# Kernel tuning notes

Hardware: AMD Instinct MI355X
Metric: run time of the kernel (lower is better)

## Reference

```python
import jax, jax.numpy as jnp
import numpy as np

KERNEL = 3
STRIDE = 1
PAD = 1


def setup_inputs() -> dict:
    key = jax.random.key(0)
    k1, k2 = jax.random.split(key)
    x = jax.random.normal(k1, (16, 32, 512, 512), dtype=jnp.float32)
    # original init: torch.rand(O, I, k, k) / (k*k)
    kernels = jax.random.uniform(k2, (32, 32, KERNEL, KERNEL), dtype=jnp.float32) / (KERNEL * KERNEL)
    return {"x": x, "kernels": kernels}


def reference(x, kernels):
    # Equivalent math to the unfold+einsum im2col conv2d: pad, extract kxk
    # windows with stride, contract over (in_channels, kh, kw).
    # Expressed as a direct convolution (cross-correlation), which is the
    # same computation without materializing the 6D window tensor.
    out = jax.lax.conv_general_dilated(
        x, kernels,
        window_strides=(STRIDE, STRIDE),
        padding=((PAD, PAD), (PAD, PAD)),
        dimension_numbers=("NCHW", "OIHW", "NCHW"),
    )
    return out  # [B, out_channels, H_out, W_out]
```

## Files before the change

kernel.cpp:

```cpp
#include <hip/hip_runtime.h>
#include <hip/hip_bf16.h>

typedef __attribute__((ext_vector_type(8))) short bf16x8;
typedef __attribute__((ext_vector_type(4))) float f32x4;
typedef __attribute__((ext_vector_type(4))) unsigned int u32x4;

#define HH 512
#define WWD 512
#define HW (HH * WWD)
#define TW 64
#define HALO_W 66
#define ROWS 10
#define NPIX (ROWS * HALO_W)
#define XBYTES (NPIX * 64)
#define WOFF XBYTES
#define WBYTES (9 * 4 * 32 * 16)
#define DUMMY (WOFF + WBYTES)
#define NITER 32

__device__ __forceinline__ unsigned short f2bf(float f) {
    unsigned u = __builtin_bit_cast(unsigned, f);
    u += 0x7FFFu + ((u >> 16) & 1u);
    return (unsigned short)(u >> 16);
}

__device__ __forceinline__ void issue4(const float* __restrict__ xb, int row0, int w0,
                                       float (&sv)[3][8]) {
    #pragma unroll
    for (int k = 0; k < 3; ++k) {
        int u = threadIdx.x + k * 512;
        int g = u / 384, r = u - g * 384, hh = r / 96, ww = r - hh * 96;
        int wwc = ww < 66 ? ww : 65;
        int row = row0 + hh, cl = w0 + wwc - 1;
        bool ok = (ww < 66) & ((unsigned)row < 512u) & ((unsigned)cl < 512u);
        int rowc = row < 0 ? 0 : (row > 511 ? 511 : row);
        int clc  = cl  < 0 ? 0 : (cl  > 511 ? 511 : cl);
        const float* src = xb + (size_t)(g * 8) * HW + rowc * WWD + clc;
        #pragma unroll
        for (int j = 0; j < 8; ++j) { float v = src[(size_t)j * HW]; sv[k][j] = ok ? v : 0.f; }
    }
}

__device__ __forceinline__ void write4(char* smem, int wsb, float (&sv)[3][8]) {
    #pragma unroll
    for (int k = 0; k < 3; ++k) {
        int u = threadIdx.x + k * 512;
        int g = u / 384, r = u - g * 384, hh = r / 96, ww = r - hh * 96;
        int slot = wsb + hh; if (slot >= ROWS) slot -= ROWS;
        int byte = (ww < 66) ? (g * NPIX + slot * HALO_W + ww) * 16
                             : (DUMMY + (threadIdx.x & 63) * 16);
        unsigned q0 = (unsigned)f2bf(sv[k][0]) | ((unsigned)f2bf(sv[k][1]) << 16);
        unsigned q1 = (unsigned)f2bf(sv[k][2]) | ((unsigned)f2bf(sv[k][3]) << 16);
        unsigned q2 = (unsigned)f2bf(sv[k][4]) | ((unsigned)f2bf(sv[k][5]) << 16);
        unsigned q3 = (unsigned)f2bf(sv[k][6]) | ((unsigned)f2bf(sv[k][7]) << 16);
        u32x4 q = { q0, q1, q2, q3 };
        *(u32x4*)(smem + byte) = q;
    }
}

template<int WAITN, bool ISS, bool WR, bool BAR>
__device__ __forceinline__ void conv_body(char* smem, const float* __restrict__ xb,
                                          float* __restrict__ ob,
                                          float (&cur)[3][8], float (&nxt)[3][8],
                                          int srb, int rowbase, int issrow, int w0,
                                          int wv, int col16, int g4) {
    if (ISS) {
        issue4(xb, issrow, w0, nxt);
        __builtin_amdgcn_sched_barrier(0);
    }
    if constexpr (WAITN == 28) asm volatile("s_waitcnt vmcnt(28)" ::: "memory");
    else if constexpr (WAITN == 4) asm volatile("s_waitcnt vmcnt(4)" ::: "memory");
    if constexpr (WAITN != 63) __builtin_amdgcn_sched_barrier(0);

    if (WR) {
        int wsb = srb + 6; if (wsb >= ROWS) wsb -= ROWS;
        write4(smem, wsb, cur);
    }

    f32x4 acc[2][2];
    {
        f32x4 z = {0.f, 0.f, 0.f, 0.f};
        acc[0][0] = z; acc[0][1] = z; acc[1][0] = z; acc[1][1] = z;
    }
    int rs[3];
    #pragma unroll
    for (int dh = 0; dh < 3; ++dh) {
        int s = srb + (wv >> 1) + dh; if (s >= ROWS) s -= ROWS;
        rs[dh] = s * HALO_W;
    }
    const int wcb = (wv & 1) * 32;
    const char* xg = smem + g4 * (NPIX * 16);
    const char* wg = smem + WOFF + g4 * 512 + col16 * 16;
    #pragma unroll
    for (int dh = 0; dh < 3; ++dh) {
        #pragma unroll
        for (int dw = 0; dw < 3; ++dw) {
            const int tap = dh * 3 + dw;
            bf16x8 b0 = *(const bf16x8*)(wg + tap * 2048);
            bf16x8 b1 = *(const bf16x8*)(wg + tap * 2048 + 256);
            #pragma unroll
            for (int m = 0; m < 2; ++m) {
                bf16x8 a = *(const bf16x8*)(xg + (rs[dh] + wcb + m * 16 + col16 + dw) * 16);
                acc[m][0] = __builtin_amdgcn_mfma_f32_16x16x32_bf16(a, b0, acc[m][0], 0, 0, 0);
                acc[m][1] = __builtin_amdgcn_mfma_f32_16x16x32_bf16(a, b1, acc[m][1], 0, 0, 0);
            }
        }
    }
    {
        float* orow = ob + (size_t)(rowbase + (wv >> 1)) * WWD + w0 + wcb;
        #pragma unroll
        for (int m = 0; m < 2; ++m)
            #pragma unroll
            for (int n = 0; n < 2; ++n)
                *(f32x4*)(orow + (size_t)(n * 16 + col16) * HW + m * 16 + g4 * 4) = acc[m][n];
    }
    if (BAR) {
        asm volatile("s_waitcnt lgkmcnt(0)" ::: "memory");
        __builtin_amdgcn_sched_barrier(0);
        __builtin_amdgcn_s_barrier();
        __builtin_amdgcn_sched_barrier(0);
    }
}

__global__ __launch_bounds__(512, 4)
void conv3x3_mfma(const float* __restrict__ x,
                  const float* __restrict__ wk,
                  float* __restrict__ out) {
    __shared__ __align__(16) char smem[DUMMY + 1024];

    const int tid   = threadIdx.x;
    const int lane  = tid & 63;
    const int wv    = tid >> 6;
    const int col16 = lane & 15;
    const int g4    = lane >> 4;

    const int w0    = blockIdx.x * TW;
    const int hbase = blockIdx.y * (4 * NITER);
    const int b     = blockIdx.z;

    const float* xb = x + (size_t)b * 32 * HW;
    float* ob = out + (size_t)b * 32 * HW;

    float svp[4][8];
    #pragma unroll
    for (int k = 0; k < 4; ++k) {
        int u = tid + k * 512;
        if (u < 1584) {
            int g = u / 396, r = u - g * 396, hh = r / 66, ww = r - hh * 66;
            int row = hbase + hh - 1, cl = w0 + ww - 1;
            bool ok = ((unsigned)row < 512u) & ((unsigned)cl < 512u);
            int rowc = row < 0 ? 0 : (row > 511 ? 511 : row);
            int clc  = cl  < 0 ? 0 : (cl  > 511 ? 511 : cl);
            const float* src = xb + (size_t)(g * 8) * HW + rowc * WWD + clc;
            #pragma unroll
            for (int j = 0; j < 8; ++j) { float v = src[(size_t)j * HW]; svp[k][j] = ok ? v : 0.f; }
        }
    }
    {
        unsigned short* wl = (unsigned short*)(smem + WOFF);
        for (int i = tid; i < 9216; i += 512) {
            int oc = i / 288; int rem = i - oc * 288;
            int ic = rem / 9; int tap = rem - ic * 9;
            wl[((tap * 4 + (ic >> 3)) * 32 + oc) * 8 + (ic & 7)] = f2bf(wk[i]);
        }
    }
    #pragma unroll
    for (int k = 0; k < 4; ++k) {
        int u = tid + k * 512;
        if (u < 1584) {
            int g = u / 396, p = u - g * 396;
            unsigned q0 = (unsigned)f2bf(svp[k][0]) | ((unsigned)f2bf(svp[k][1]) << 16);
            unsigned q1 = (unsigned)f2bf(svp[k][2]) | ((unsigned)f2bf(svp[k][3]) << 16);
            unsigned q2 = (unsigned)f2bf(svp[k][4]) | ((unsigned)f2bf(svp[k][5]) << 16);
            unsigned q3 = (unsigned)f2bf(svp[k][6]) | ((unsigned)f2bf(svp[k][7]) << 16);
            u32x4 q = { q0, q1, q2, q3 };
            *(u32x4*)(smem + (g * NPIX + p) * 16) = q;
        }
    }

    float svA[3][8], svB[3][8];
    issue4(xb, hbase + 5, w0, svA);
    __builtin_amdgcn_sched_barrier(0);
    __syncthreads();

    int srb = 0;
    conv_body<28, 1, 1, 1>(smem, xb, ob, svA, svB, srb, hbase, hbase + 9, w0, wv, col16, g4);
    srb = 4;
    #pragma unroll 1
    for (int tp = 0; tp < 14; ++tp) {
        int t1 = 1 + 2 * tp;
        conv_body<28, 1, 1, 1>(smem, xb, ob, svB, svA, srb,
                               hbase + 4 * t1, hbase + 4 * t1 + 9, w0, wv, col16, g4);
        srb += 4; if (srb >= ROWS) srb -= ROWS;
        conv_body<28, 1, 1, 1>(smem, xb, ob, svA, svB, srb,
                               hbase + 4 * (t1 + 1), hbase + 4 * (t1 + 1) + 9, w0, wv, col16, g4);
        srb += 4; if (srb >= ROWS) srb -= ROWS;
    }
    conv_body<28, 1, 1, 1>(smem, xb, ob, svB, svA, srb, hbase + 116, hbase + 125, w0, wv, col16, g4);
    srb += 4; if (srb >= ROWS) srb -= ROWS;
    conv_body<4, 0, 1, 1>(smem, xb, ob, svA, svB, srb, hbase + 120, 0, w0, wv, col16, g4);
    srb += 4; if (srb >= ROWS) srb -= ROWS;
    conv_body<63, 0, 0, 0>(smem, xb, ob, svB, svA, srb, hbase + 124, 0, w0, wv, col16, g4);
}

extern "C" void kernel_launch(void* const* d_in, const int* in_sizes, int n_in,
                              void* d_out, int out_size, void* d_ws, size_t ws_size,
                              hipStream_t stream) {
    const float* x  = (const float*)d_in[0];
    const float* wk = (const float*)d_in[1];
    float* out = (float*)d_out;
    dim3 grid(WWD / TW, HH / (4 * NITER), 16);
    conv3x3_mfma<<<grid, 512, 0, stream>>>(x, wk, out);
}
```

Before: 278.4 us.

## Hold conv weights in registers and tighten halo row loading

Weight fragments for all nine taps are now built once per block into registers, which removes the per-tap weight reads from LDS in the inner MFMA loop and frees the LDS weight region. The halo row load now uses a tighter thread-to-pixel mapping with 68-wide rows and fewer idle lanes. The LDS write of the previous row block now happens before the next global loads are issued, with a single vmcnt(4) wait. This adds 72 VGPRs of weight data per thread under launch bounds of 512x4, which risks register pressure or spills, and it changes how much load latency the pipeline can hide.

```diff
diff --git a/kernel.cpp b/kernel.cpp
--- a/kernel.cpp
+++ b/kernel.cpp
@@ -13,9 +13,7 @@
 #define ROWS 10
 #define NPIX (ROWS * HALO_W)
 #define XBYTES (NPIX * 64)
-#define WOFF XBYTES
-#define WBYTES (9 * 4 * 32 * 16)
-#define DUMMY (WOFF + WBYTES)
+#define DUMMY XBYTES
 #define NITER 32
 
 __device__ __forceinline__ unsigned short f2bf(float f) {
@@ -28,8 +26,9 @@
                                        float (&sv)[3][8]) {
     #pragma unroll
     for (int k = 0; k < 3; ++k) {
-        int u = threadIdx.x + k * 512;
-        int g = u / 384, r = u - g * 384, hh = r / 96, ww = r - hh * 96;
+        if (k == 2 && threadIdx.x >= 64) continue;
+        int u = (k < 2) ? (int)threadIdx.x + k * 512 : 1024 + (int)(threadIdx.x & 63);
+        int g = u / 272, r = u - g * 272, hh = r / 68, ww = r - hh * 68;
         int wwc = ww < 66 ? ww : 65;
         int row = row0 + hh, cl = w0 + wwc - 1;
         bool ok = (ww < 66) & ((unsigned)row < 512u) & ((unsigned)cl < 512u);
@@ -44,8 +43,9 @@
 __device__ __forceinline__ void write4(char* smem, int wsb, float (&sv)[3][8]) {
     #pragma unroll
     for (int k = 0; k < 3; ++k) {
-        int u = threadIdx.x + k * 512;
-        int g = u / 384, r = u - g * 384, hh = r / 96, ww = r - hh * 96;
+        if (k == 2 && threadIdx.x >= 64) continue;
+        int u = (k < 2) ? (int)threadIdx.x + k * 512 : 1024 + (int)(threadIdx.x & 63);
+        int g = u / 272, r = u - g * 272, hh = r / 68, ww = r - hh * 68;
         int slot = wsb + hh; if (slot >= ROWS) slot -= ROWS;
         int byte = (ww < 66) ? (g * NPIX + slot * HALO_W + ww) * 16
                              : (DUMMY + (threadIdx.x & 63) * 16);
@@ -58,24 +58,19 @@
     }
 }
 
-template<int WAITN, bool ISS, bool WR, bool BAR>
+template<bool WR, bool ISS, bool BAR>
 __device__ __forceinline__ void conv_body(char* smem, const float* __restrict__ xb,
-                                          float* __restrict__ ob,
+                                          float* __restrict__ ob, bf16x8 (&wf)[9][2],
                                           float (&cur)[3][8], float (&nxt)[3][8],
                                           int srb, int rowbase, int issrow, int w0,
                                           int wv, int col16, int g4) {
-    if (ISS) {
-        issue4(xb, issrow, w0, nxt);
+    if (WR) {
+        asm volatile("s_waitcnt vmcnt(4)" ::: "memory");
         __builtin_amdgcn_sched_barrier(0);
-    }
-    if constexpr (WAITN == 28) asm volatile("s_waitcnt vmcnt(28)" ::: "memory");
-    else if constexpr (WAITN == 4) asm volatile("s_waitcnt vmcnt(4)" ::: "memory");
-    if constexpr (WAITN != 63) __builtin_amdgcn_sched_barrier(0);
-
-    if (WR) {
         int wsb = srb + 6; if (wsb >= ROWS) wsb -= ROWS;
         write4(smem, wsb, cur);
     }
+    if (ISS) issue4(xb, issrow, w0, nxt);
 
     f32x4 acc[2][2];
     {
@@ -90,19 +85,16 @@
     }
     const int wcb = (wv & 1) * 32;
     const char* xg = smem + g4 * (NPIX * 16);
-    const char* wg = smem + WOFF + g4 * 512 + col16 * 16;
     #pragma unroll
     for (int dh = 0; dh < 3; ++dh) {
         #pragma unroll
         for (int dw = 0; dw < 3; ++dw) {
             const int tap = dh * 3 + dw;
-            bf16x8 b0 = *(const bf16x8*)(wg + tap * 2048);
-            bf16x8 b1 = *(const bf16x8*)(wg + tap * 2048 + 256);
             #pragma unroll
             for (int m = 0; m < 2; ++m) {
                 bf16x8 a = *(const bf16x8*)(xg + (rs[dh] + wcb + m * 16 + col16 + dw) * 16);
-                acc[m][0] = __builtin_amdgcn_mfma_f32_16x16x32_bf16(a, b0, acc[m][0], 0, 0, 0);
-                acc[m][1] = __builtin_amdgcn_mfma_f32_16x16x32_bf16(a, b1, acc[m][1], 0, 0, 0);
+                acc[m][0] = __builtin_amdgcn_mfma_f32_16x16x32_bf16(a, wf[tap][0], acc[m][0], 0, 0, 0);
+                acc[m][1] = __builtin_amdgcn_mfma_f32_16x16x32_bf16(a, wf[tap][1], acc[m][1], 0, 0, 0);
             }
         }
     }
@@ -126,7 +118,7 @@
 void conv3x3_mfma(const float* __restrict__ x,
                   const float* __restrict__ wk,
                   float* __restrict__ out) {
-    __shared__ __align__(16) char smem[DUMMY + 1024];
+    __shared__ __align__(16) char smem[XBYTES + 1024];
 
     const int tid   = threadIdx.x;
     const int lane  = tid & 63;
@@ -141,40 +133,56 @@
     const float* xb = x + (size_t)b * 32 * HW;
     float* ob = out + (size_t)b * 32 * HW;
 
-    float svp[4][8];
-    #pragma unroll
-    for (int k = 0; k < 4; ++k) {
-        int u = tid + k * 512;
-        if (u < 1584) {
-            int g = u / 396, r = u - g * 396, hh = r / 66, ww = r - hh * 66;
-            int row = hbase + hh - 1, cl = w0 + ww - 1;
-            bool ok = ((unsigned)row < 512u) & ((unsigned)cl < 512u);
-            int rowc = row < 0 ? 0 : (row > 511 ? 511 : row);
-            int clc  = cl  < 0 ? 0 : (cl  > 511 ? 511 : cl);
-            const float* src = xb + (size_t)(g * 8) * HW + rowc * WWD + clc;
+    bf16x8 wf[9][2];
+    {
+        float* ws = (float*)smem;
+        for (int i = tid; i < 9216; i += 512) {
+            int oc = i / 288;
+            ws[oc * 289 + (i - oc * 288)] = wk[i];
+        }
+        __syncthreads();
+        #pragma unroll
+        for (int tap = 0; tap < 9; ++tap) {
             #pragma unroll
-            for (int j = 0; j < 8; ++j) { float v = src[(size_t)j * HW]; svp[k][j] = ok ? v : 0.f; }
-        }
-    }
-    {
-        unsigned short* wl = (unsigned short*)(smem + WOFF);
-        for (int i = tid; i < 9216; i += 512) {
-            int oc = i / 288; int rem = i - oc * 288;
-            int ic = rem / 9; int tap = rem - ic * 9;
-            wl[((tap * 4 + (ic >> 3)) * 32 + oc) * 8 + (ic & 7)] = f2bf(wk[i]);
-        }
-    }
-    #pragma unroll
-    for (int k = 0; k < 4; ++k) {
-        int u = tid + k * 512;
-        if (u < 1584) {
-            int g = u / 396, p = u - g * 396;
-            unsigned q0 = (unsigned)f2bf(svp[k][0]) | ((unsigned)f2bf(svp[k][1]) << 16);
-            unsigned q1 = (unsigned)f2bf(svp[k][2]) | ((unsigned)f2bf(svp[k][3]) << 16);
-            unsigned q2 = (unsigned)f2bf(svp[k][4]) | ((unsigned)f2bf(svp[k][5]) << 16);
-            unsigned q3 = (unsigned)f2bf(svp[k][6]) | ((unsigned)f2bf(svp[k][7]) << 16);
-            u32x4 q = { q0, q1, q2, q3 };
-            *(u32x4*)(smem + (g * NPIX + p) * 16) = q;
+            for (int n = 0; n < 2; ++n) {
+                bf16x8 f;
+                #pragma unroll
+                for (int j = 0; j < 8; ++j)
+                    f[j] = (short)f2bf(ws[(n * 16 + col16) * 289 + (g4 * 8 + j) * 9 + tap]);
+                wf[tap][n] = f;
+            }
+        }
+        __syncthreads();
+    }
+
+    {
+        float svp[4][8];
+        #pragma unroll
+        for (int k = 0; k < 4; ++k) {
+            int u = tid + k * 512;
+            if (u < 1584) {
+                int g = u / 396, r = u - g * 396, hh = r / 66, ww = r - hh * 66;
+                int row = hbase + hh - 1, cl = w0 + ww - 1;
+                bool ok = ((unsigned)row < 512u) & ((unsigned)cl < 512u);
+                int rowc = row < 0 ? 0 : (row > 511 ? 511 : row);
+                int clc  = cl  < 0 ? 0 : (cl  > 511 ? 511 : cl);
+                const float* src = xb + (size_t)(g * 8) * HW + rowc * WWD + clc;
+                #pragma unroll
+                for (int j = 0; j < 8; ++j) { float v = src[(size_t)j * HW]; svp[k][j] = ok ? v : 0.f; }
+            }
+        }
+        #pragma unroll
+        for (int k = 0; k < 4; ++k) {
+            int u = tid + k * 512;
+            if (u < 1584) {
+                int g = u / 396, p = u - g * 396;
+                unsigned q0 = (unsigned)f2bf(svp[k][0]) | ((unsigned)f2bf(svp[k][1]) << 16);
+                unsigned q1 = (unsigned)f2bf(svp[k][2]) | ((unsigned)f2bf(svp[k][3]) << 16);
+                unsigned q2 = (unsigned)f2bf(svp[k][4]) | ((unsigned)f2bf(svp[k][5]) << 16);
+                unsigned q3 = (unsigned)f2bf(svp[k][6]) | ((unsigned)f2bf(svp[k][7]) << 16);
+                u32x4 q = { q0, q1, q2, q3 };
+                *(u32x4*)(smem + (g * NPIX + p) * 16) = q;
+            }
         }
     }
 
@@ -184,23 +192,23 @@
     __syncthreads();
 
     int srb = 0;
-    conv_body<28, 1, 1, 1>(smem, xb, ob, svA, svB, srb, hbase, hbase + 9, w0, wv, col16, g4);
+    conv_body<1, 1, 1>(smem, xb, ob, wf, svA, svB, srb, hbase, hbase + 9, w0, wv, col16, g4);
     srb = 4;
     #pragma unroll 1
     for (int tp = 0; tp < 14; ++tp) {
         int t1 = 1 + 2 * tp;
-        conv_body<28, 1, 1, 1>(smem, xb, ob, svB, svA, srb,
-                               hbase + 4 * t1, hbase + 4 * t1 + 9, w0, wv, col16, g4);
+        conv_body<1, 1, 1>(smem, xb, ob, wf, svB, svA, srb,
+                           hbase + 4 * t1, hbase + 4 * t1 + 9, w0, wv, col16, g4);
         srb += 4; if (srb >= ROWS) srb -= ROWS;
-        conv_body<28, 1, 1, 1>(smem, xb, ob, svA, svB, srb,
-                               hbase + 4 * (t1 + 1), hbase + 4 * (t1 + 1) + 9, w0, wv, col16, g4);
+        conv_body<1, 1, 1>(smem, xb, ob, wf, svA, svB, srb,
+                           hbase + 4 * (t1 + 1), hbase + 4 * (t1 + 1) + 9, w0, wv, col16, g4);
         srb += 4; if (srb >= ROWS) srb -= ROWS;
     }
-    conv_body<28, 1, 1, 1>(smem, xb, ob, svB, svA, srb, hbase + 116, hbase + 125, w0, wv, col16, g4);
+    conv_body<1, 1, 1>(smem, xb, ob, wf, svB, svA, srb, hbase + 116, hbase + 125, w0, wv, col16, g4);
     srb += 4; if (srb >= ROWS) srb -= ROWS;
-    conv_body<4, 0, 1, 1>(smem, xb, ob, svA, svB, srb, hbase + 120, 0, w0, wv, col16, g4);
+    conv_body<1, 0, 1>(smem, xb, ob, wf, svA, svB, srb, hbase + 120, 0, w0, wv, col16, g4);
     srb += 4; if (srb >= ROWS) srb -= ROWS;
-    conv_body<63, 0, 0, 0>(smem, xb, ob, svB, svA, srb, hbase + 124, 0, w0, wv, col16, g4);
+    conv_body<0, 0, 0>(smem, xb, ob, wf, svB, svA, srb, hbase + 124, 0, w0, wv, col16, g4);
 }
 
 extern "C" void kernel_launch(void* const* d_in, const int* in_sizes, int n_in,
```

New measurement: 958.5 us. 244% more time.

## Shrink blocks to 256 threads with 2-row steps and 6-slot ring buffer

Applied to the files above, without the earlier changes.

Reworks the rolling halo pipeline so each block has 4 waves and computes 2 output rows per step instead of 4. Shared memory holds 6 row slots instead of 10, and the grid doubles along height. The prefetch is now issued after the shared-memory write, with one vmcnt wait per step, so loads overlap the MFMA compute of the next step. The aim is more resident blocks and smaller shared memory per block. In exchange, halo rows are re-read more often, weights are reloaded per block, and there are more barriers per output row.

```diff
diff --git a/kernel.cpp b/kernel.cpp
--- a/kernel.cpp
+++ b/kernel.cpp
@@ -9,13 +9,11 @@
 #define WWD 512
 #define HW (HH * WWD)
 #define TW 64
-#define HALO_W 66
-#define ROWS 10
-#define NPIX (ROWS * HALO_W)
-#define XBYTES (NPIX * 64)
+#define SLOTS 6
+#define PXG (SLOTS * 66)
+#define XBYTES (4 * PXG * 16)
 #define WOFF XBYTES
-#define WBYTES (9 * 4 * 32 * 16)
-#define DUMMY (WOFF + WBYTES)
+#define DUMMY (WOFF + 18432)
 #define NITER 32
 
 __device__ __forceinline__ unsigned short f2bf(float f) {
@@ -24,12 +22,13 @@
     return (unsigned short)(u >> 16);
 }
 
-__device__ __forceinline__ void issue4(const float* __restrict__ xb, int row0, int w0,
+__device__ __forceinline__ void issue2(const float* __restrict__ xb, int row0, int w0,
                                        float (&sv)[3][8]) {
     #pragma unroll
     for (int k = 0; k < 3; ++k) {
-        int u = threadIdx.x + k * 512;
-        int g = u / 384, r = u - g * 384, hh = r / 96, ww = r - hh * 96;
+        if (k == 2 && threadIdx.x >= 32) continue;
+        int u = (k < 2) ? (int)threadIdx.x + k * 256 : 512 + (int)threadIdx.x;
+        int g = u / 136, r = u - g * 136, hh = r / 68, ww = r - hh * 68;
         int wwc = ww < 66 ? ww : 65;
         int row = row0 + hh, cl = w0 + wwc - 1;
         bool ok = (ww < 66) & ((unsigned)row < 512u) & ((unsigned)cl < 512u);
@@ -41,13 +40,14 @@
     }
 }
 
-__device__ __forceinline__ void write4(char* smem, int wsb, float (&sv)[3][8]) {
+__device__ __forceinline__ void write2(char* smem, int wsb, float (&sv)[3][8]) {
     #pragma unroll
     for (int k = 0; k < 3; ++k) {
-        int u = threadIdx.x + k * 512;
-        int g = u / 384, r = u - g * 384, hh = r / 96, ww = r - hh * 96;
-        int slot = wsb + hh; if (slot >= ROWS) slot -= ROWS;
-        int byte = (ww < 66) ? (g * NPIX + slot * HALO_W + ww) * 16
+        if (k == 2 && threadIdx.x >= 32) continue;
+        int u = (k < 2) ? (int)threadIdx.x + k * 256 : 512 + (int)threadIdx.x;
+        int g = u / 136, r = u - g * 136, hh = r / 68, ww = r - hh * 68;
+        int slot = wsb + hh; if (slot >= SLOTS) slot -= SLOTS;
+        int byte = (ww < 66) ? (g * PXG + slot * 66 + ww) * 16
                              : (DUMMY + (threadIdx.x & 63) * 16);
         unsigned q0 = (unsigned)f2bf(sv[k][0]) | ((unsigned)f2bf(sv[k][1]) << 16);
         unsigned q1 = (unsigned)f2bf(sv[k][2]) | ((unsigned)f2bf(sv[k][3]) << 16);
@@ -58,24 +58,19 @@
     }
 }
 
-template<int WAITN, bool ISS, bool WR, bool BAR>
+template<bool WR, bool ISS, bool BAR>
 __device__ __forceinline__ void conv_body(char* smem, const float* __restrict__ xb,
                                           float* __restrict__ ob,
                                           float (&cur)[3][8], float (&nxt)[3][8],
                                           int srb, int rowbase, int issrow, int w0,
                                           int wv, int col16, int g4) {
-    if (ISS) {
-        issue4(xb, issrow, w0, nxt);
+    if (WR) {
+        asm volatile("s_waitcnt vmcnt(4)" ::: "memory");
         __builtin_amdgcn_sched_barrier(0);
-    }
-    if constexpr (WAITN == 28) asm volatile("s_waitcnt vmcnt(28)" ::: "memory");
-    else if constexpr (WAITN == 4) asm volatile("s_waitcnt vmcnt(4)" ::: "memory");
-    if constexpr (WAITN != 63) __builtin_amdgcn_sched_barrier(0);
-
-    if (WR) {
-        int wsb = srb + 6; if (wsb >= ROWS) wsb -= ROWS;
-        write4(smem, wsb, cur);
-    }
+        int wsb = srb + 4; if (wsb >= SLOTS) wsb -= SLOTS;
+        write2(smem, wsb, cur);
+    }
+    if (ISS) issue2(xb, issrow, w0, nxt);
 
     f32x4 acc[2][2];
     {
@@ -85,11 +80,11 @@
     int rs[3];
     #pragma unroll
     for (int dh = 0; dh < 3; ++dh) {
-        int s = srb + (wv >> 1) + dh; if (s >= ROWS) s -= ROWS;
-        rs[dh] = s * HALO_W;
-    }
-    const int wcb = (wv & 1) * 32;
-    const char* xg = smem + g4 * (NPIX * 16);
+        int s = srb + (wv & 1) + dh; if (s >= SLOTS) s -= SLOTS;
+        rs[dh] = s * 66;
+    }
+    const int wcb = (wv >> 1) * 32;
+    const char* xg = smem + g4 * (PXG * 16);
     const char* wg = smem + WOFF + g4 * 512 + col16 * 16;
     #pragma unroll
     for (int dh = 0; dh < 3; ++dh) {
@@ -107,7 +102,7 @@
         }
     }
     {
-        float* orow = ob + (size_t)(rowbase + (wv >> 1)) * WWD + w0 + wcb;
+        float* orow = ob + (size_t)(rowbase + (wv & 1)) * WWD + w0 + wcb;
         #pragma unroll
         for (int m = 0; m < 2; ++m)
             #pragma unroll
@@ -122,7 +117,7 @@
     }
 }
 
-__global__ __launch_bounds__(512, 4)
+__global__ __launch_bounds__(256, 3)
 void conv3x3_mfma(const float* __restrict__ x,
                   const float* __restrict__ wk,
                   float* __restrict__ out) {
@@ -135,18 +130,28 @@
     const int g4    = lane >> 4;
 
     const int w0    = blockIdx.x * TW;
-    const int hbase = blockIdx.y * (4 * NITER);
+    const int hbase = blockIdx.y * (2 * NITER);
     const int b     = blockIdx.z;
 
     const float* xb = x + (size_t)b * 32 * HW;
     float* ob = out + (size_t)b * 32 * HW;
 
-    float svp[4][8];
-    #pragma unroll
-    for (int k = 0; k < 4; ++k) {
-        int u = tid + k * 512;
-        if (u < 1584) {
-            int g = u / 396, r = u - g * 396, hh = r / 66, ww = r - hh * 66;
+    {
+        unsigned short* wl = (unsigned short*)(smem + WOFF);
+        for (int i = tid; i < 9216; i += 256) {
+            int oc = i / 288; int rem = i - oc * 288;
+            int ic = rem / 9; int tap = rem - ic * 9;
+            wl[((tap * 4 + (ic >> 3)) * 32 + oc) * 8 + (ic & 7)] = f2bf(wk[i]);
+        }
+    }
+
+    {
+        float svp[5][8];
+        #pragma unroll
+        for (int k = 0; k < 5; ++k) {
+            if (k == 4 && tid >= 32) continue;
+            int u = (k < 4) ? tid + k * 256 : 1024 + tid;
+            int g = u / 264, p = u - g * 264, hh = p / 66, ww = p - hh * 66;
             int row = hbase + hh - 1, cl = w0 + ww - 1;
             bool ok = ((unsigned)row < 512u) & ((unsigned)cl < 512u);
             int rowc = row < 0 ? 0 : (row > 511 ? 511 : row);
@@ -155,52 +160,43 @@
             #pragma unroll
             for (int j = 0; j < 8; ++j) { float v = src[(size_t)j * HW]; svp[k][j] = ok ? v : 0.f; }
         }
-    }
-    {
-        unsigned short* wl = (unsigned short*)(smem + WOFF);
-        for (int i = tid; i < 9216; i += 512) {
-            int oc = i / 288; int rem = i - oc * 288;
-            int ic = rem / 9; int tap = rem - ic * 9;
-            wl[((tap * 4 + (ic >> 3)) * 32 + oc) * 8 + (ic & 7)] = f2bf(wk[i]);
-        }
-    }
-    #pragma unroll
-    for (int k = 0; k < 4; ++k) {
-        int u = tid + k * 512;
-        if (u < 1584) {
-            int g = u / 396, p = u - g * 396;
+        #pragma unroll
+        for (int k = 0; k < 5; ++k) {
+            if (k == 4 && tid >= 32) continue;
+            int u = (k < 4) ? tid + k * 256 : 1024 + tid;
+            int g = u / 264, p = u - g * 264;
             unsigned q0 = (unsigned)f2bf(svp[k][0]) | ((unsigned)f2bf(svp[k][1]) << 16);
             unsigned q1 = (unsigned)f2bf(svp[k][2]) | ((unsigned)f2bf(svp[k][3]) << 16);
             unsigned q2 = (unsigned)f2bf(svp[k][4]) | ((unsigned)f2bf(svp[k][5]) << 16);
             unsigned q3 = (unsigned)f2bf(svp[k][6]) | ((unsigned)f2bf(svp[k][7]) << 16);
             u32x4 q = { q0, q1, q2, q3 };
-            *(u32x4*)(smem + (g * NPIX + p) * 16) = q;
+            *(u32x4*)(smem + (g * PXG + p) * 16) = q;
         }
     }
 
     float svA[3][8], svB[3][8];
-    issue4(xb, hbase + 5, w0, svA);
+    issue2(xb, hbase + 3, w0, svA);
     __builtin_amdgcn_sched_barrier(0);
     __syncthreads();
 
     int srb = 0;
-    conv_body<28, 1, 1, 1>(smem, xb, ob, svA, svB, srb, hbase, hbase + 9, w0, wv, col16, g4);
-    srb = 4;
+    conv_body<1, 1, 1>(smem, xb, ob, svA, svB, 0, hbase, hbase + 5, w0, wv, col16, g4);
+    srb = 2;
     #pragma unroll 1
     for (int tp = 0; tp < 14; ++tp) {
         int t1 = 1 + 2 * tp;
-        conv_body<28, 1, 1, 1>(smem, xb, ob, svB, svA, srb,
-                               hbase + 4 * t1, hbase + 4 * t1 + 9, w0, wv, col16, g4);
-        srb += 4; if (srb >= ROWS) srb -= ROWS;
-        conv_body<28, 1, 1, 1>(smem, xb, ob, svA, svB, srb,
-                               hbase + 4 * (t1 + 1), hbase + 4 * (t1 + 1) + 9, w0, wv, col16, g4);
-        srb += 4; if (srb >= ROWS) srb -= ROWS;
-    }
-    conv_body<28, 1, 1, 1>(smem, xb, ob, svB, svA, srb, hbase + 116, hbase + 125, w0, wv, col16, g4);
-    srb += 4; if (srb >= ROWS) srb -= ROWS;
-    conv_body<4, 0, 1, 1>(smem, xb, ob, svA, svB, srb, hbase + 120, 0, w0, wv, col16, g4);
-    srb += 4; if (srb >= ROWS) srb -= ROWS;
-    conv_body<63, 0, 0, 0>(smem, xb, ob, svB, svA, srb, hbase + 124, 0, w0, wv, col16, g4);
+        conv_body<1, 1, 1>(smem, xb, ob, svB, svA, srb,
+                           hbase + 2 * t1, hbase + 2 * t1 + 5, w0, wv, col16, g4);
+        srb += 2; if (srb >= SLOTS) srb -= SLOTS;
+        conv_body<1, 1, 1>(smem, xb, ob, svA, svB, srb,
+                           hbase + 2 * (t1 + 1), hbase + 2 * (t1 + 1) + 5, w0, wv, col16, g4);
+        srb += 2; if (srb >= SLOTS) srb -= SLOTS;
+    }
+    conv_body<1, 1, 1>(smem, xb, ob, svB, svA, srb, hbase + 58, hbase + 63, w0, wv, col16, g4);
+    srb += 2; if (srb >= SLOTS) srb -= SLOTS;
+    conv_body<1, 0, 1>(smem, xb, ob, svA, svB, srb, hbase + 60, 0, w0, wv, col16, g4);
+    srb += 2; if (srb >= SLOTS) srb -= SLOTS;
+    conv_body<0, 0, 0>(smem, xb, ob, svB, svA, srb, hbase + 62, 0, w0, wv, col16, g4);
 }
 
 extern "C" void kernel_launch(void* const* d_in, const int* in_sizes, int n_in,
@@ -209,6 +205,6 @@
     const float* x  = (const float*)d_in[0];
     const float* wk = (const float*)d_in[1];
     float* out = (float*)d_out;
-    dim3 grid(WWD / TW, HH / (4 * NITER), 16);
-    conv3x3_mfma<<<grid, 512, 0, stream>>>(x, wk, out);
-}
+    dim3 grid(WWD / TW, HH / (2 * NITER), 16);
+    conv3x3_mfma<<<grid, 256, 0, stream>>>(x, wk, out);
+}
```

Measured after the change: 286.8 us. 3.0% more time.
